# Performance work log

Measured on AMD Instinct MI355X. Metric: run time of the kernel, lower is better.

The kernel has to match this reference:

```python
import jax, jax.numpy as jnp
from jax import lax
import numpy as np

RADIUS = 0.2   # ball-query radius (module init arg)
NSAMPLE = 32   # gather_size
STRIDE = 4     # npoint = ceil(N / STRIDE)


def setup_inputs() -> dict:
    key = jax.random.key(0)
    k1, k2, k3 = jax.random.split(key, 3)
    points = jax.random.uniform(k1, (4, 8192, 3), jnp.float32)      # (B,N,3) in unit cube
    features = jax.random.normal(k2, (4, 8192, 64), jnp.float32)    # (B,N,C)
    # Conv2d(in=C+3, out=128, kernel=(1, NSAMPLE), bias=False) weight
    weight = jax.random.normal(k3, (128, 67, 1, 32), jnp.float32) * 0.02
    return {"points": points, "features": features, "weight": weight}


def fps(xyz, npoint):
    """Furthest point sampling. xyz: (B,N,3) -> inds (B,npoint) int32."""
    B, N, _ = xyz.shape
    start = jnp.zeros((B,), jnp.int32)          # standard FPS starts at index 0
    dist0 = jnp.full((B, N), 1e10, xyz.dtype)

    def body(carry, _):
        dist, last = carry
        last_xyz = jnp.take_along_axis(xyz, last[:, None, None], axis=1)  # (B,1,3)
        d = jnp.sum((xyz - last_xyz) ** 2, axis=-1)                        # (B,N)
        dist = jnp.minimum(dist, d)
        nxt = jnp.argmax(dist, axis=-1).astype(jnp.int32)
        return (dist, nxt), nxt

    (_, _), rest = lax.scan(body, (dist0, start), None, length=npoint - 1)
    return jnp.concatenate([start[None, :], rest], axis=0).T  # (B,npoint)


def ball_query(xyz, new_xyz, radius, nsample):
    """For each center, first `nsample` point indices within radius, padded with
    the first valid index (pointnet2 semantics). Returns (B,npoint,nsample)."""
    N = xyz.shape[1]
    d2 = jnp.sum((new_xyz[:, :, None, :] - xyz[:, None, :, :]) ** 2, axis=-1)  # (B,npoint,N)
    cand = jnp.where(d2 < radius * radius, jnp.arange(N, dtype=jnp.int32), N)
    neg, _ = lax.top_k(-cand, nsample)   # smallest nsample indices, in order
    idx = -neg
    first = idx[..., :1]                 # center itself is always in-ball -> valid
    return jnp.where(idx == N, first, idx)


def _forward(points, features, weight):
    B, N, _ = points.shape
    npoint = (N + STRIDE - 1) // STRIDE
    inds = fps(points, npoint)                                        # (B,npoint)
    new_xyz = jnp.take_along_axis(points, inds[..., None], axis=1)    # (B,npoint,3)
    idx = ball_query(points, new_xyz, RADIUS, NSAMPLE)                # (B,npoint,nsample)

    gather = lambda v: jax.vmap(lambda a, i: a[i])(v, idx)            # (B,npoint,nsample,*)
    g_xyz = gather(points) - new_xyz[:, :, None, :]                   # relative coords
    g_feat = gather(features)
    g = jnp.concatenate([g_xyz, g_feat], axis=-1)                     # (B,npoint,nsample,3+C)

    # Conv2d with kernel (1,nsample): contract over channel + neighbor axes.
    conv = jnp.einsum("bpsc,ocs->bpo", g, weight[:, :, 0, :])         # (B,npoint,Cout)
    return new_xyz, conv


def reference(points, features, weight):
    return _forward(points, features, weight)
```

## Files before the change

kernel.cpp:

```cpp
#include <hip/hip_runtime.h>

#define BATCH   4
#define NPTS    8192
#define NPOINT  2048
#define NSAMPLE 32
#define NCH     67
#define NOUT    128
#define NP      4
#define FPS_T   512
#define NWAVE   (FPS_T / 64)
#define KPT     (NPTS / FPS_T)
#define NBKT    64

#define DPP_ROW_SHR1    0x111
#define DPP_ROW_SHR2    0x112
#define DPP_ROW_SHR4    0x114
#define DPP_ROW_SHR8    0x118
#define DPP_ROW_BCAST15 0x142
#define DPP_ROW_BCAST31 0x143

#define DPP_MAX_HOP(key, ctrl)                                                 \
    {                                                                          \
        int _lo = (int)(unsigned)(key);                                        \
        int _hi = (int)(unsigned)((key) >> 32);                                \
        int _olo = __builtin_amdgcn_update_dpp(0, _lo, (ctrl), 0xF, 0xF, true);\
        int _ohi = __builtin_amdgcn_update_dpp(0, _hi, (ctrl), 0xF, 0xF, true);\
        unsigned long long _o =                                                \
            ((unsigned long long)(unsigned)_ohi << 32) | (unsigned)_olo;       \
        if (_o > (key)) (key) = _o;                                            \
    }

#define DPP_REDUCE_MAX(key)            \
    DPP_MAX_HOP(key, DPP_ROW_SHR1);    \
    DPP_MAX_HOP(key, DPP_ROW_SHR2);    \
    DPP_MAX_HOP(key, DPP_ROW_SHR4);    \
    DPP_MAX_HOP(key, DPP_ROW_SHR8);    \
    DPP_MAX_HOP(key, DPP_ROW_BCAST15); \
    DPP_MAX_HOP(key, DPP_ROW_BCAST31);

__global__ __launch_bounds__(FPS_T) void fps_kernel(
    const float* __restrict__ points, float* __restrict__ new_xyz)
{
#pragma clang fp contract(off)
    const int b    = blockIdx.x;
    const int t    = threadIdx.x;
    const int lane = t & 63;
    const int w    = t >> 6;
    const float* pts = points + (size_t)b * NPTS * 3;

    __shared__ float2 xy[NPTS];
    __shared__ float2 zd[NPTS];
    __shared__ unsigned short orig16[NPTS];
    __shared__ unsigned long long key_g[2][NBKT];
    __shared__ int start[NBKT + 1];
    __shared__ int cursor[NBKT];
    __shared__ float bbr[6][NWAVE];

    float mnx = 1e30f, mny = 1e30f, mnz = 1e30f;
    float mxx = -1e30f, mxy = -1e30f, mxz = -1e30f;
    for (int k = 0; k < KPT; ++k) {
        const int i = k * FPS_T + t;
        float xx = pts[3 * i], yy = pts[3 * i + 1], zz = pts[3 * i + 2];
        mnx = fminf(mnx, xx); mxx = fmaxf(mxx, xx);
        mny = fminf(mny, yy); mxy = fmaxf(mxy, yy);
        mnz = fminf(mnz, zz); mxz = fmaxf(mxz, zz);
    }
#pragma unroll
    for (int off = 32; off >= 1; off >>= 1) {
        mnx = fminf(mnx, __shfl_down(mnx, off));
        mny = fminf(mny, __shfl_down(mny, off));
        mnz = fminf(mnz, __shfl_down(mnz, off));
        mxx = fmaxf(mxx, __shfl_down(mxx, off));
        mxy = fmaxf(mxy, __shfl_down(mxy, off));
        mxz = fmaxf(mxz, __shfl_down(mxz, off));
    }
    if (lane == 0) {
        bbr[0][w] = mnx; bbr[1][w] = mny; bbr[2][w] = mnz;
        bbr[3][w] = mxx; bbr[4][w] = mxy; bbr[5][w] = mxz;
    }
    if (t < NBKT) cursor[t] = 0;
    __syncthreads();
    mnx = bbr[0][0]; mny = bbr[1][0]; mnz = bbr[2][0];
    mxx = bbr[3][0]; mxy = bbr[4][0]; mxz = bbr[5][0];
#pragma unroll
    for (int q = 1; q < NWAVE; ++q) {
        mnx = fminf(mnx, bbr[0][q]); mny = fminf(mny, bbr[1][q]);
        mnz = fminf(mnz, bbr[2][q]); mxx = fmaxf(mxx, bbr[3][q]);
        mxy = fmaxf(mxy, bbr[4][q]); mxz = fmaxf(mxz, bbr[5][q]);
    }
    const float rx = mxx - mnx, ry = mxy - mny, rz = mxz - mnz;
    const float sclx = (rx > 0.f) ? 4.0f / rx : 0.f;
    const float scly = (ry > 0.f) ? 4.0f / ry : 0.f;
    const float sclz = (rz > 0.f) ? 4.0f / rz : 0.f;

    for (int k = 0; k < KPT; ++k) {
        const int i = k * FPS_T + t;
        float xx = pts[3 * i], yy = pts[3 * i + 1], zz = pts[3 * i + 2];
        int cxi = min(3, max(0, (int)((xx - mnx) * sclx)));
        int cyi = min(3, max(0, (int)((yy - mny) * scly)));
        int czi = min(3, max(0, (int)((zz - mnz) * sclz)));
        atomicAdd(&cursor[cxi | (cyi << 2) | (czi << 4)], 1);
    }
    __syncthreads();
    if (t == 0) {
        int acc = 0;
        for (int g = 0; g < NBKT; ++g) { start[g] = acc; acc += cursor[g]; }
        start[NBKT] = acc;
    }
    __syncthreads();
    const int vs0 = start[lane];
    const int vln = start[lane + 1] - vs0;
    if (t < NBKT) cursor[t] = start[t];
    __syncthreads();

    for (int k = 0; k < KPT; ++k) {
        const int i = k * FPS_T + t;
        float xx = pts[3 * i], yy = pts[3 * i + 1], zz = pts[3 * i + 2];
        int cxi = min(3, max(0, (int)((xx - mnx) * sclx)));
        int cyi = min(3, max(0, (int)((yy - mny) * scly)));
        int czi = min(3, max(0, (int)((zz - mnz) * sclz)));
        int slot = atomicAdd(&cursor[cxi | (cyi << 2) | (czi << 4)], 1);
        xy[slot] = make_float2(xx, yy);
        zd[slot] = make_float2(zz, 10000000000.0f);
        orig16[slot] = (unsigned short)i;
    }

    const float cwx = rx * 0.25f, cwy = ry * 0.25f, cwz = rz * 0.25f;
    const float bxl = mnx + (float)(lane & 3) * cwx,        bxh = bxl + cwx;
    const float byl = mny + (float)((lane >> 2) & 3) * cwy, byh = byl + cwy;
    const float bzl = mnz + (float)((lane >> 4) & 3) * cwz, bzh = bzl + cwz;
    const unsigned long long below = (1ull << lane) - 1ull;

    float cx = pts[0], cy = pts[1], cz = pts[2];
    if (t == 0) {
        float* o = new_xyz + (size_t)b * NPOINT * 3;
        o[0] = cx; o[1] = cy; o[2] = cz;
    }
    unsigned long long kk =
        ((unsigned long long)__float_as_uint(10000000000.0f) << 32);
    __syncthreads();

    for (int it = 1; it < NPOINT; ++it) {
        const int par = it & 1;

        float ddx = fmaxf(fmaxf(bxl - cx, cx - bxh), 0.0f);
        float ddy = fmaxf(fmaxf(byl - cy, cy - byh), 0.0f);
        float ddz = fmaxf(fmaxf(bzl - cz, cz - bzh), 0.0f);
        float dmin2 = ddx * ddx + ddy * ddy + ddz * ddz;
        float ub = __uint_as_float((unsigned)(kk >> 32));
        bool scan = dmin2 < ub * 1.0001f + 1e-5f;
        unsigned long long m = __ballot(scan);

        const int rank = (int)__popcll(m & below);
        const bool mine = scan && ((rank & (NWAVE - 1)) == w);
        unsigned long long mw = __ballot(mine);

        while (mw) {
            const int g = __ffsll((long long)mw) - 1;
            mw &= mw - 1;
            const int s0 = __builtin_amdgcn_readlane(vs0, g);
            const int ln = __builtin_amdgcn_readlane(vln, g);
            unsigned long long bk = 0;
            for (int jo = lane; jo < ln; jo += 64) {
                const int j = s0 + jo;
                float2 vxy = xy[j];
                float2 vzd = zd[j];
                float dx = vxy.x - cx;
                float dy = vxy.y - cy;
                float dz = vzd.x - cz;
                float d  = ((dx * dx) + (dy * dy)) + (dz * dz);
                float nd = fminf(vzd.y, d);
                zd[j].y = nd;
                unsigned long long kkey =
                    ((unsigned long long)__float_as_uint(nd) << 32)
                  | ((unsigned)(8191 - (int)orig16[j]) << 13)
                  | (unsigned)j;
                if (kkey > bk) bk = kkey;
            }
            DPP_REDUCE_MAX(bk);
            if (lane == 63) key_g[par][g] = bk;
        }
        __syncthreads();

        if (scan) kk = key_g[par][lane];
        unsigned long long rr = kk;
        DPP_REDUCE_MAX(rr);
        const unsigned rlo =
            (unsigned)__builtin_amdgcn_readlane((int)(unsigned)rr, 63);
        const int slot = (int)(rlo & 0x1FFFu);
        float2 wxy = xy[slot];
        float2 wzd = zd[slot];
        cx = wxy.x; cy = wxy.y; cz = wzd.x;
        if (t == 0) {
            float* o = new_xyz + ((size_t)b * NPOINT + it) * 3;
            o[0] = cx; o[1] = cy; o[2] = cz;
        }
    }
}

__global__ __launch_bounds__(256) void ballq_kernel(
    const float* __restrict__ points, const float* __restrict__ new_xyz,
    int* __restrict__ ballidx)
{
#pragma clang fp contract(off)
    const int wid  = (int)((blockIdx.x * 256 + threadIdx.x) >> 6);
    const int lane = threadIdx.x & 63;
    const int b = wid / NPOINT;
    const float* ctr = new_xyz + (size_t)wid * 3;
    const float cx = ctr[0], cy = ctr[1], cz = ctr[2];
    const float* pts = points + (size_t)b * NPTS * 3;
    int* out = ballidx + (size_t)wid * NSAMPLE;
    const float r2 = (float)(0.2 * 0.2);

    int cnt = 0;
    int first = 0;
    bool havefirst = false;
    for (int base = 0; base < NPTS && cnt < NSAMPLE; base += 64) {
        const int j = base + lane;
        float dx = pts[3 * j + 0] - cx;
        float dy = pts[3 * j + 1] - cy;
        float dz = pts[3 * j + 2] - cz;
        float d2 = ((dx * dx) + (dy * dy)) + (dz * dz);
        const bool in = d2 < r2;
        unsigned long long m = __ballot(in);
        if (in) {
            int pos = cnt + __popcll(m & ((1ull << lane) - 1ull));
            if (pos < NSAMPLE) out[pos] = j;
        }
        if (!havefirst && m != 0ull) {
            first = base + (__ffsll((long long)m) - 1);
            havefirst = true;
        }
        cnt += __popcll(m);
    }
    if (lane >= cnt && lane < NSAMPLE) out[lane] = first;
}

__global__ __launch_bounds__(128) void conv_kernel(
    const float* __restrict__ points, const float* __restrict__ features,
    const float* __restrict__ weight, const float* __restrict__ new_xyz,
    const int* __restrict__ ballidx, float* __restrict__ conv_out)
{
    __shared__ float g[NP][NCH][NSAMPLE];
    const int t = threadIdx.x;
    const int bp0 = blockIdx.x * NP;
    const int b = bp0 / NPOINT;
    const float* pts = points + (size_t)b * NPTS * 3;
    const float* fts = features + (size_t)b * NPTS * 64;

    {
        const int p = t >> 5;
        const int s = t & 31;
        const int ci = bp0 + p;
        const int j = ballidx[(size_t)ci * NSAMPLE + s];
        const float* ctr = new_xyz + (size_t)ci * 3;
        const float* pj = pts + 3 * j;
        g[p][0][s] = pj[0] - ctr[0];
        g[p][1][s] = pj[1] - ctr[1];
        g[p][2][s] = pj[2] - ctr[2];
        const float4* fj = (const float4*)(fts + (size_t)j * 64);
#pragma unroll
        for (int c4 = 0; c4 < 16; ++c4) {
            float4 v = fj[c4];
            g[p][3 + 4 * c4 + 0][s] = v.x;
            g[p][3 + 4 * c4 + 1][s] = v.y;
            g[p][3 + 4 * c4 + 2][s] = v.z;
            g[p][3 + 4 * c4 + 3][s] = v.w;
        }
    }
    __syncthreads();

    const int o = t;
    float acc0 = 0.f, acc1 = 0.f, acc2 = 0.f, acc3 = 0.f;
    const float* wr = weight + (size_t)o * NCH * NSAMPLE;
    for (int c = 0; c < NCH; ++c) {
        const float4* w4 = (const float4*)(wr + c * NSAMPLE);
#pragma unroll
        for (int s4 = 0; s4 < 8; ++s4) {
            float4 wv = w4[s4];
            float4 g0 = *(const float4*)&g[0][c][s4 * 4];
            float4 g1 = *(const float4*)&g[1][c][s4 * 4];
            float4 g2 = *(const float4*)&g[2][c][s4 * 4];
            float4 g3 = *(const float4*)&g[3][c][s4 * 4];
            acc0 += g0.x * wv.x + g0.y * wv.y + g0.z * wv.z + g0.w * wv.w;
            acc1 += g1.x * wv.x + g1.y * wv.y + g1.z * wv.z + g1.w * wv.w;
            acc2 += g2.x * wv.x + g2.y * wv.y + g2.z * wv.z + g2.w * wv.w;
            acc3 += g3.x * wv.x + g3.y * wv.y + g3.z * wv.z + g3.w * wv.w;
        }
    }
    float* outp = conv_out + (size_t)bp0 * NOUT;
    outp[0 * NOUT + o] = acc0;
    outp[1 * NOUT + o] = acc1;
    outp[2 * NOUT + o] = acc2;
    outp[3 * NOUT + o] = acc3;
}

extern "C" void kernel_launch(void* const* d_in, const int* in_sizes, int n_in,
                              void* d_out, int out_size, void* d_ws, size_t ws_size,
                              hipStream_t stream)
{
    const float* points   = (const float*)d_in[0];
    const float* features = (const float*)d_in[1];
    const float* weight   = (const float*)d_in[2];

    float* new_xyz = (float*)d_out;
    float* conv    = (float*)d_out + (size_t)BATCH * NPOINT * 3;

    int* ballidx = (int*)d_ws;

    fps_kernel<<<BATCH, FPS_T, 0, stream>>>(points, new_xyz);
    ballq_kernel<<<(BATCH * NPOINT * 64) / 256, 256, 0, stream>>>(points, new_xyz, ballidx);
    conv_kernel<<<(BATCH * NPOINT) / NP, 128, 0, stream>>>(points, features, weight, new_xyz, ballidx, conv);
}
```

Measured before the change: 2.018 ms.

## Fuse FPS, ball query and conv into one persistent kernel with progress flags

Merges the three kernels into a single persistent launch. Four blocks run furthest point sampling and publish progress counters every 16 centers. The remaining blocks pull tickets and spin on those counters, so ball query and conv for finished centers overlap with the sequential FPS loop. Ball indices now stay in shared memory instead of a global workspace. The cost is a spin-wait protocol that relies on all blocks being co-resident and on correct release/acquire ordering, plus a memset launch.

```diff
diff --git a/kernel.cpp b/kernel.cpp
--- a/kernel.cpp
+++ b/kernel.cpp
@@ -6,11 +6,14 @@
 #define NSAMPLE 32
 #define NCH     67
 #define NOUT    128
-#define NP      4
 #define FPS_T   512
 #define NWAVE   (FPS_T / 64)
 #define KPT     (NPTS / FPS_T)
 #define NBKT    64
+#define NFPS    4
+#define NBLK    256
+#define TPT     8
+#define NTICK   (BATCH * NPOINT / TPT)
 
 #define DPP_ROW_SHR1    0x111
 #define DPP_ROW_SHR2    0x112
@@ -38,261 +41,277 @@
     DPP_MAX_HOP(key, DPP_ROW_BCAST15); \
     DPP_MAX_HOP(key, DPP_ROW_BCAST31);
 
-__global__ __launch_bounds__(FPS_T) void fps_kernel(
-    const float* __restrict__ points, float* __restrict__ new_xyz)
+__global__ __launch_bounds__(FPS_T) void fused_kernel(
+    const float* __restrict__ points, const float* __restrict__ features,
+    const float* __restrict__ weight, float* __restrict__ new_xyz,
+    float* __restrict__ conv_out, int* __restrict__ ctl)
 {
-#pragma clang fp contract(off)
-    const int b    = blockIdx.x;
+    __shared__ __attribute__((aligned(16))) char smem[149504];
     const int t    = threadIdx.x;
     const int lane = t & 63;
     const int w    = t >> 6;
-    const float* pts = points + (size_t)b * NPTS * 3;
-
-    __shared__ float2 xy[NPTS];
-    __shared__ float2 zd[NPTS];
-    __shared__ unsigned short orig16[NPTS];
-    __shared__ unsigned long long key_g[2][NBKT];
-    __shared__ int start[NBKT + 1];
-    __shared__ int cursor[NBKT];
-    __shared__ float bbr[6][NWAVE];
-
-    float mnx = 1e30f, mny = 1e30f, mnz = 1e30f;
-    float mxx = -1e30f, mxy = -1e30f, mxz = -1e30f;
-    for (int k = 0; k < KPT; ++k) {
-        const int i = k * FPS_T + t;
-        float xx = pts[3 * i], yy = pts[3 * i + 1], zz = pts[3 * i + 2];
-        mnx = fminf(mnx, xx); mxx = fmaxf(mxx, xx);
-        mny = fminf(mny, yy); mxy = fmaxf(mxy, yy);
-        mnz = fminf(mnz, zz); mxz = fmaxf(mxz, zz);
+    int* prog = ctl;
+    int* ticket = ctl + 32;
+
+    if (blockIdx.x < NFPS) {
+#pragma clang fp contract(off)
+        const int b = blockIdx.x;
+        const float* pts = points + (size_t)b * NPTS * 3;
+
+        float2* xy = (float2*)smem;
+        float2* zd = (float2*)(smem + 65536);
+        unsigned short* orig16 = (unsigned short*)(smem + 131072);
+        unsigned long long (*key_g)[NBKT] =
+            (unsigned long long (*)[NBKT])(smem + 147456);
+        int* start  = (int*)(smem + 148480);
+        int* cursor = (int*)(smem + 148744);
+        float (*bbr)[NWAVE] = (float (*)[NWAVE])(smem + 149000);
+
+        float mnx = 1e30f, mny = 1e30f, mnz = 1e30f;
+        float mxx = -1e30f, mxy = -1e30f, mxz = -1e30f;
+        for (int k = 0; k < KPT; ++k) {
+            const int i = k * FPS_T + t;
+            float xx = pts[3 * i], yy = pts[3 * i + 1], zz = pts[3 * i + 2];
+            mnx = fminf(mnx, xx); mxx = fmaxf(mxx, xx);
+            mny = fminf(mny, yy); mxy = fmaxf(mxy, yy);
+            mnz = fminf(mnz, zz); mxz = fmaxf(mxz, zz);
+        }
+#pragma unroll
+        for (int off = 32; off >= 1; off >>= 1) {
+            mnx = fminf(mnx, __shfl_down(mnx, off));
+            mny = fminf(mny, __shfl_down(mny, off));
+            mnz = fminf(mnz, __shfl_down(mnz, off));
+            mxx = fmaxf(mxx, __shfl_down(mxx, off));
+            mxy = fmaxf(mxy, __shfl_down(mxy, off));
+            mxz = fmaxf(mxz, __shfl_down(mxz, off));
+        }
+        if (lane == 0) {
+            bbr[0][w] = mnx; bbr[1][w] = mny; bbr[2][w] = mnz;
+            bbr[3][w] = mxx; bbr[4][w] = mxy; bbr[5][w] = mxz;
+        }
+        if (t < NBKT) cursor[t] = 0;
+        __syncthreads();
+        mnx = bbr[0][0]; mny = bbr[1][0]; mnz = bbr[2][0];
+        mxx = bbr[3][0]; mxy = bbr[4][0]; mxz = bbr[5][0];
+#pragma unroll
+        for (int q = 1; q < NWAVE; ++q) {
+            mnx = fminf(mnx, bbr[0][q]); mny = fminf(mny, bbr[1][q]);
+            mnz = fminf(mnz, bbr[2][q]); mxx = fmaxf(mxx, bbr[3][q]);
+            mxy = fmaxf(mxy, bbr[4][q]); mxz = fmaxf(mxz, bbr[5][q]);
+        }
+        const float rx = mxx - mnx, ry = mxy - mny, rz = mxz - mnz;
+        const float sclx = (rx > 0.f) ? 4.0f / rx : 0.f;
+        const float scly = (ry > 0.f) ? 4.0f / ry : 0.f;
+        const float sclz = (rz > 0.f) ? 4.0f / rz : 0.f;
+
+        for (int k = 0; k < KPT; ++k) {
+            const int i = k * FPS_T + t;
+            float xx = pts[3 * i], yy = pts[3 * i + 1], zz = pts[3 * i + 2];
+            int cxi = min(3, max(0, (int)((xx - mnx) * sclx)));
+            int cyi = min(3, max(0, (int)((yy - mny) * scly)));
+            int czi = min(3, max(0, (int)((zz - mnz) * sclz)));
+            atomicAdd(&cursor[cxi | (cyi << 2) | (czi << 4)], 1);
+        }
+        __syncthreads();
+        if (t == 0) {
+            int acc = 0;
+            for (int g = 0; g < NBKT; ++g) { start[g] = acc; acc += cursor[g]; }
+            start[NBKT] = acc;
+        }
+        __syncthreads();
+        const int vs0 = start[lane];
+        const int vln = start[lane + 1] - vs0;
+        if (t < NBKT) cursor[t] = start[t];
+        __syncthreads();
+
+        for (int k = 0; k < KPT; ++k) {
+            const int i = k * FPS_T + t;
+            float xx = pts[3 * i], yy = pts[3 * i + 1], zz = pts[3 * i + 2];
+            int cxi = min(3, max(0, (int)((xx - mnx) * sclx)));
+            int cyi = min(3, max(0, (int)((yy - mny) * scly)));
+            int czi = min(3, max(0, (int)((zz - mnz) * sclz)));
+            int slot = atomicAdd(&cursor[cxi | (cyi << 2) | (czi << 4)], 1);
+            xy[slot] = make_float2(xx, yy);
+            zd[slot] = make_float2(zz, 10000000000.0f);
+            orig16[slot] = (unsigned short)i;
+        }
+
+        const float cwx = rx * 0.25f, cwy = ry * 0.25f, cwz = rz * 0.25f;
+        const float bxl = mnx + (float)(lane & 3) * cwx,        bxh = bxl + cwx;
+        const float byl = mny + (float)((lane >> 2) & 3) * cwy, byh = byl + cwy;
+        const float bzl = mnz + (float)((lane >> 4) & 3) * cwz, bzh = bzl + cwz;
+        const unsigned long long below = (1ull << lane) - 1ull;
+
+        float cx = pts[0], cy = pts[1], cz = pts[2];
+        if (t == 0) {
+            float* o = new_xyz + (size_t)b * NPOINT * 3;
+            o[0] = cx; o[1] = cy; o[2] = cz;
+        }
+        unsigned long long kk =
+            ((unsigned long long)__float_as_uint(10000000000.0f) << 32);
+        __syncthreads();
+
+        for (int it = 1; it < NPOINT; ++it) {
+            const int par = it & 1;
+            float ddx = fmaxf(fmaxf(bxl - cx, cx - bxh), 0.0f);
+            float ddy = fmaxf(fmaxf(byl - cy, cy - byh), 0.0f);
+            float ddz = fmaxf(fmaxf(bzl - cz, cz - bzh), 0.0f);
+            float dmin2 = ddx * ddx + ddy * ddy + ddz * ddz;
+            float ub = __uint_as_float((unsigned)(kk >> 32));
+            bool scan = dmin2 < ub * 1.0001f + 1e-5f;
+            unsigned long long m = __ballot(scan);
+
+            const int rank = (int)__popcll(m & below);
+            const bool mine = scan && ((rank & (NWAVE - 1)) == w);
+            unsigned long long mw = __ballot(mine);
+
+            while (mw) {
+                const int g = __ffsll((long long)mw) - 1;
+                mw &= mw - 1;
+                const int s0 = __builtin_amdgcn_readlane(vs0, g);
+                const int ln = __builtin_amdgcn_readlane(vln, g);
+                unsigned long long bk = 0;
+                for (int jo = lane; jo < ln; jo += 64) {
+                    const int j = s0 + jo;
+                    float2 vxy = xy[j];
+                    float2 vzd = zd[j];
+                    float dx = vxy.x - cx;
+                    float dy = vxy.y - cy;
+                    float dz = vzd.x - cz;
+                    float d  = ((dx * dx) + (dy * dy)) + (dz * dz);
+                    float nd = fminf(vzd.y, d);
+                    zd[j].y = nd;
+                    unsigned long long kkey =
+                        ((unsigned long long)__float_as_uint(nd) << 32)
+                      | ((unsigned)(8191 - (int)orig16[j]) << 13)
+                      | (unsigned)j;
+                    if (kkey > bk) bk = kkey;
+                }
+                DPP_REDUCE_MAX(bk);
+                if (lane == 63) key_g[par][g] = bk;
+            }
+            __syncthreads();
+
+            if (scan) kk = key_g[par][lane];
+            unsigned long long rr = kk;
+            DPP_REDUCE_MAX(rr);
+            const unsigned rlo =
+                (unsigned)__builtin_amdgcn_readlane((int)(unsigned)rr, 63);
+            const int slot = (int)(rlo & 0x1FFFu);
+            float2 wxy = xy[slot];
+            float2 wzd = zd[slot];
+            cx = wxy.x; cy = wxy.y; cz = wzd.x;
+            if (t == 0) {
+                float* o = new_xyz + ((size_t)b * NPOINT + it) * 3;
+                o[0] = cx; o[1] = cy; o[2] = cz;
+                if (((it & 15) == 15) || (it == NPOINT - 1)) {
+                    __threadfence();
+                    __hip_atomic_store(&prog[b], it + 1, __ATOMIC_RELEASE,
+                                       __HIP_MEMORY_SCOPE_AGENT);
+                }
+            }
+        }
+        return;
     }
+
+    float (*g)[NCH][NSAMPLE] = (float (*)[NCH][NSAMPLE])smem;
+    int (*idx)[NSAMPLE] = (int (*)[NSAMPLE])(smem + 68608);
+    int* tk_s = (int*)(smem + 69632);
+
+    for (;;) {
+        if (t == 0) *tk_s = atomicAdd(ticket, 1);
+        __syncthreads();
+        const int T = *tk_s;
+        __syncthreads();
+        if (T >= NTICK) break;
+        const int b   = T & 3;
+        const int it0 = (T >> 2) * TPT;
+
+        if (t == 0) {
+            while (__hip_atomic_load(&prog[b], __ATOMIC_ACQUIRE,
+                                     __HIP_MEMORY_SCOPE_AGENT) < it0 + TPT)
+                __builtin_amdgcn_s_sleep(8);
+        }
+        __syncthreads();
+
+        const float* pts = points + (size_t)b * NPTS * 3;
+        const float* fts = features + (size_t)b * NPTS * 64;
+
+        {
+#pragma clang fp contract(off)
+            const int gci = b * NPOINT + it0 + w;
+            const float cx = new_xyz[3 * gci + 0];
+            const float cy = new_xyz[3 * gci + 1];
+            const float cz = new_xyz[3 * gci + 2];
+            const float r2 = (float)(0.2 * 0.2);
+            int* out = idx[w];
+            int cnt = 0, first = 0;
+            bool havefirst = false;
+            for (int base = 0; base < NPTS && cnt < NSAMPLE; base += 64) {
+                const int j = base + lane;
+                float dx = pts[3 * j + 0] - cx;
+                float dy = pts[3 * j + 1] - cy;
+                float dz = pts[3 * j + 2] - cz;
+                float d2 = ((dx * dx) + (dy * dy)) + (dz * dz);
+                const bool in = d2 < r2;
+                unsigned long long m = __ballot(in);
+                if (in) {
+                    int pos = cnt + __popcll(m & ((1ull << lane) - 1ull));
+                    if (pos < NSAMPLE) out[pos] = j;
+                }
+                if (!havefirst && m != 0ull) {
+                    first = base + (__ffsll((long long)m) - 1);
+                    havefirst = true;
+                }
+                cnt += __popcll(m);
+            }
+            if (lane >= cnt && lane < NSAMPLE) out[lane] = first;
+        }
+        __syncthreads();
+
+        if (t < TPT * NSAMPLE) {
+            const int p = t >> 5;
+            const int s = t & 31;
+            const int gci = b * NPOINT + it0 + p;
+            const int j = idx[p][s];
+            const float* pj = pts + 3 * j;
+            g[p][0][s] = pj[0] - new_xyz[3 * gci + 0];
+            g[p][1][s] = pj[1] - new_xyz[3 * gci + 1];
+            g[p][2][s] = pj[2] - new_xyz[3 * gci + 2];
+            const float4* fj = (const float4*)(fts + (size_t)j * 64);
 #pragma unroll
-    for (int off = 32; off >= 1; off >>= 1) {
-        mnx = fminf(mnx, __shfl_down(mnx, off));
-        mny = fminf(mny, __shfl_down(mny, off));
-        mnz = fminf(mnz, __shfl_down(mnz, off));
-        mxx = fmaxf(mxx, __shfl_down(mxx, off));
-        mxy = fmaxf(mxy, __shfl_down(mxy, off));
-        mxz = fmaxf(mxz, __shfl_down(mxz, off));
+            for (int c4 = 0; c4 < 16; ++c4) {
+                float4 v = fj[c4];
+                g[p][3 + 4 * c4 + 0][s] = v.x;
+                g[p][3 + 4 * c4 + 1][s] = v.y;
+                g[p][3 + 4 * c4 + 2][s] = v.z;
+                g[p][3 + 4 * c4 + 3][s] = v.w;
+            }
+        }
+        __syncthreads();
+
+        {
+            const int o = t & 127;
+            const int q = t >> 7;
+            float acc0 = 0.f, acc1 = 0.f;
+            const float* wr = weight + (size_t)o * NCH * NSAMPLE;
+            for (int c = 0; c < NCH; ++c) {
+                const float4* w4 = (const float4*)(wr + c * NSAMPLE);
+#pragma unroll
+                for (int s4 = 0; s4 < 8; ++s4) {
+                    float4 wv = w4[s4];
+                    float4 g0 = *(const float4*)&g[q][c][s4 * 4];
+                    float4 g1 = *(const float4*)&g[q + 4][c][s4 * 4];
+                    acc0 += g0.x * wv.x + g0.y * wv.y + g0.z * wv.z + g0.w * wv.w;
+                    acc1 += g1.x * wv.x + g1.y * wv.y + g1.z * wv.z + g1.w * wv.w;
+                }
+            }
+            float* outp = conv_out + ((size_t)b * NPOINT + it0) * NOUT;
+            outp[(q    ) * NOUT + o] = acc0;
+            outp[(q + 4) * NOUT + o] = acc1;
+        }
+        __syncthreads();
     }
-    if (lane == 0) {
-        bbr[0][w] = mnx; bbr[1][w] = mny; bbr[2][w] = mnz;
-        bbr[3][w] = mxx; bbr[4][w] = mxy; bbr[5][w] = mxz;
-    }
-    if (t < NBKT) cursor[t] = 0;
-    __syncthreads();
-    mnx = bbr[0][0]; mny = bbr[1][0]; mnz = bbr[2][0];
-    mxx = bbr[3][0]; mxy = bbr[4][0]; mxz = bbr[5][0];
-#pragma unroll
-    for (int q = 1; q < NWAVE; ++q) {
-        mnx = fminf(mnx, bbr[0][q]); mny = fminf(mny, bbr[1][q]);
-        mnz = fminf(mnz, bbr[2][q]); mxx = fmaxf(mxx, bbr[3][q]);
-        mxy = fmaxf(mxy, bbr[4][q]); mxz = fmaxf(mxz, bbr[5][q]);
-    }
-    const float rx = mxx - mnx, ry = mxy - mny, rz = mxz - mnz;
-    const float sclx = (rx > 0.f) ? 4.0f / rx : 0.f;
-    const float scly = (ry > 0.f) ? 4.0f / ry : 0.f;
-    const float sclz = (rz > 0.f) ? 4.0f / rz : 0.f;
-
-    for (int k = 0; k < KPT; ++k) {
-        const int i = k * FPS_T + t;
-        float xx = pts[3 * i], yy = pts[3 * i + 1], zz = pts[3 * i + 2];
-        int cxi = min(3, max(0, (int)((xx - mnx) * sclx)));
-        int cyi = min(3, max(0, (int)((yy - mny) * scly)));
-        int czi = min(3, max(0, (int)((zz - mnz) * sclz)));
-        atomicAdd(&cursor[cxi | (cyi << 2) | (czi << 4)], 1);
-    }
-    __syncthreads();
-    if (t == 0) {
-        int acc = 0;
-        for (int g = 0; g < NBKT; ++g) { start[g] = acc; acc += cursor[g]; }
-        start[NBKT] = acc;
-    }
-    __syncthreads();
-    const int vs0 = start[lane];
-    const int vln = start[lane + 1] - vs0;
-    if (t < NBKT) cursor[t] = start[t];
-    __syncthreads();
-
-    for (int k = 0; k < KPT; ++k) {
-        const int i = k * FPS_T + t;
-        float xx = pts[3 * i], yy = pts[3 * i + 1], zz = pts[3 * i + 2];
-        int cxi = min(3, max(0, (int)((xx - mnx) * sclx)));
-        int cyi = min(3, max(0, (int)((yy - mny) * scly)));
-        int czi = min(3, max(0, (int)((zz - mnz) * sclz)));
-        int slot = atomicAdd(&cursor[cxi | (cyi << 2) | (czi << 4)], 1);
-        xy[slot] = make_float2(xx, yy);
-        zd[slot] = make_float2(zz, 10000000000.0f);
-        orig16[slot] = (unsigned short)i;
-    }
-
-    const float cwx = rx * 0.25f, cwy = ry * 0.25f, cwz = rz * 0.25f;
-    const float bxl = mnx + (float)(lane & 3) * cwx,        bxh = bxl + cwx;
-    const float byl = mny + (float)((lane >> 2) & 3) * cwy, byh = byl + cwy;
-    const float bzl = mnz + (float)((lane >> 4) & 3) * cwz, bzh = bzl + cwz;
-    const unsigned long long below = (1ull << lane) - 1ull;
-
-    float cx = pts[0], cy = pts[1], cz = pts[2];
-    if (t == 0) {
-        float* o = new_xyz + (size_t)b * NPOINT * 3;
-        o[0] = cx; o[1] = cy; o[2] = cz;
-    }
-    unsigned long long kk =
-        ((unsigned long long)__float_as_uint(10000000000.0f) << 32);
-    __syncthreads();
-
-    for (int it = 1; it < NPOINT; ++it) {
-        const int par = it & 1;
-
-        float ddx = fmaxf(fmaxf(bxl - cx, cx - bxh), 0.0f);
-        float ddy = fmaxf(fmaxf(byl - cy, cy - byh), 0.0f);
-        float ddz = fmaxf(fmaxf(bzl - cz, cz - bzh), 0.0f);
-        float dmin2 = ddx * ddx + ddy * ddy + ddz * ddz;
-        float ub = __uint_as_float((unsigned)(kk >> 32));
-        bool scan = dmin2 < ub * 1.0001f + 1e-5f;
-        unsigned long long m = __ballot(scan);
-
-        const int rank = (int)__popcll(m & below);
-        const bool mine = scan && ((rank & (NWAVE - 1)) == w);
-        unsigned long long mw = __ballot(mine);
-
-        while (mw) {
-            const int g = __ffsll((long long)mw) - 1;
-            mw &= mw - 1;
-            const int s0 = __builtin_amdgcn_readlane(vs0, g);
-            const int ln = __builtin_amdgcn_readlane(vln, g);
-            unsigned long long bk = 0;
-            for (int jo = lane; jo < ln; jo += 64) {
-                const int j = s0 + jo;
-                float2 vxy = xy[j];
-                float2 vzd = zd[j];
-                float dx = vxy.x - cx;
-                float dy = vxy.y - cy;
-                float dz = vzd.x - cz;
-                float d  = ((dx * dx) + (dy * dy)) + (dz * dz);
-                float nd = fminf(vzd.y, d);
-                zd[j].y = nd;
-                unsigned long long kkey =
-                    ((unsigned long long)__float_as_uint(nd) << 32)
-                  | ((unsigned)(8191 - (int)orig16[j]) << 13)
-                  | (unsigned)j;
-                if (kkey > bk) bk = kkey;
-            }
-            DPP_REDUCE_MAX(bk);
-            if (lane == 63) key_g[par][g] = bk;
-        }
-        __syncthreads();
-
-        if (scan) kk = key_g[par][lane];
-        unsigned long long rr = kk;
-        DPP_REDUCE_MAX(rr);
-        const unsigned rlo =
-            (unsigned)__builtin_amdgcn_readlane((int)(unsigned)rr, 63);
-        const int slot = (int)(rlo & 0x1FFFu);
-        float2 wxy = xy[slot];
-        float2 wzd = zd[slot];
-        cx = wxy.x; cy = wxy.y; cz = wzd.x;
-        if (t == 0) {
-            float* o = new_xyz + ((size_t)b * NPOINT + it) * 3;
-            o[0] = cx; o[1] = cy; o[2] = cz;
-        }
-    }
-}
-
-__global__ __launch_bounds__(256) void ballq_kernel(
-    const float* __restrict__ points, const float* __restrict__ new_xyz,
-    int* __restrict__ ballidx)
-{
-#pragma clang fp contract(off)
-    const int wid  = (int)((blockIdx.x * 256 + threadIdx.x) >> 6);
-    const int lane = threadIdx.x & 63;
-    const int b = wid / NPOINT;
-    const float* ctr = new_xyz + (size_t)wid * 3;
-    const float cx = ctr[0], cy = ctr[1], cz = ctr[2];
-    const float* pts = points + (size_t)b * NPTS * 3;
-    int* out = ballidx + (size_t)wid * NSAMPLE;
-    const float r2 = (float)(0.2 * 0.2);
-
-    int cnt = 0;
-    int first = 0;
-    bool havefirst = false;
-    for (int base = 0; base < NPTS && cnt < NSAMPLE; base += 64) {
-        const int j = base + lane;
-        float dx = pts[3 * j + 0] - cx;
-        float dy = pts[3 * j + 1] - cy;
-        float dz = pts[3 * j + 2] - cz;
-        float d2 = ((dx * dx) + (dy * dy)) + (dz * dz);
-        const bool in = d2 < r2;
-        unsigned long long m = __ballot(in);
-        if (in) {
-            int pos = cnt + __popcll(m & ((1ull << lane) - 1ull));
-            if (pos < NSAMPLE) out[pos] = j;
-        }
-        if (!havefirst && m != 0ull) {
-            first = base + (__ffsll((long long)m) - 1);
-            havefirst = true;
-        }
-        cnt += __popcll(m);
-    }
-    if (lane >= cnt && lane < NSAMPLE) out[lane] = first;
-}
-
-__global__ __launch_bounds__(128) void conv_kernel(
-    const float* __restrict__ points, const float* __restrict__ features,
-    const float* __restrict__ weight, const float* __restrict__ new_xyz,
-    const int* __restrict__ ballidx, float* __restrict__ conv_out)
-{
-    __shared__ float g[NP][NCH][NSAMPLE];
-    const int t = threadIdx.x;
-    const int bp0 = blockIdx.x * NP;
-    const int b = bp0 / NPOINT;
-    const float* pts = points + (size_t)b * NPTS * 3;
-    const float* fts = features + (size_t)b * NPTS * 64;
-
-    {
-        const int p = t >> 5;
-        const int s = t & 31;
-        const int ci = bp0 + p;
-        const int j = ballidx[(size_t)ci * NSAMPLE + s];
-        const float* ctr = new_xyz + (size_t)ci * 3;
-        const float* pj = pts + 3 * j;
-        g[p][0][s] = pj[0] - ctr[0];
-        g[p][1][s] = pj[1] - ctr[1];
-        g[p][2][s] = pj[2] - ctr[2];
-        const float4* fj = (const float4*)(fts + (size_t)j * 64);
-#pragma unroll
-        for (int c4 = 0; c4 < 16; ++c4) {
-            float4 v = fj[c4];
-            g[p][3 + 4 * c4 + 0][s] = v.x;
-            g[p][3 + 4 * c4 + 1][s] = v.y;
-            g[p][3 + 4 * c4 + 2][s] = v.z;
-            g[p][3 + 4 * c4 + 3][s] = v.w;
-        }
-    }
-    __syncthreads();
-
-    const int o = t;
-    float acc0 = 0.f, acc1 = 0.f, acc2 = 0.f, acc3 = 0.f;
-    const float* wr = weight + (size_t)o * NCH * NSAMPLE;
-    for (int c = 0; c < NCH; ++c) {
-        const float4* w4 = (const float4*)(wr + c * NSAMPLE);
-#pragma unroll
-        for (int s4 = 0; s4 < 8; ++s4) {
-            float4 wv = w4[s4];
-            float4 g0 = *(const float4*)&g[0][c][s4 * 4];
-            float4 g1 = *(const float4*)&g[1][c][s4 * 4];
-            float4 g2 = *(const float4*)&g[2][c][s4 * 4];
-            float4 g3 = *(const float4*)&g[3][c][s4 * 4];
-            acc0 += g0.x * wv.x + g0.y * wv.y + g0.z * wv.z + g0.w * wv.w;
-            acc1 += g1.x * wv.x + g1.y * wv.y + g1.z * wv.z + g1.w * wv.w;
-            acc2 += g2.x * wv.x + g2.y * wv.y + g2.z * wv.z + g2.w * wv.w;
-            acc3 += g3.x * wv.x + g3.y * wv.y + g3.z * wv.z + g3.w * wv.w;
-        }
-    }
-    float* outp = conv_out + (size_t)bp0 * NOUT;
-    outp[0 * NOUT + o] = acc0;
-    outp[1 * NOUT + o] = acc1;
-    outp[2 * NOUT + o] = acc2;
-    outp[3 * NOUT + o] = acc3;
 }
 
 extern "C" void kernel_launch(void* const* d_in, const int* in_sizes, int n_in,
@@ -305,10 +324,9 @@
 
     float* new_xyz = (float*)d_out;
     float* conv    = (float*)d_out + (size_t)BATCH * NPOINT * 3;
-
-    int* ballidx = (int*)d_ws;
-
-    fps_kernel<<<BATCH, FPS_T, 0, stream>>>(points, new_xyz);
-    ballq_kernel<<<(BATCH * NPOINT * 64) / 256, 256, 0, stream>>>(points, new_xyz, ballidx);
-    conv_kernel<<<(BATCH * NPOINT) / NP, 128, 0, stream>>>(points, features, weight, new_xyz, ballidx, conv);
+    int* ctl = (int*)d_ws;
+
+    hipMemsetAsync(d_ws, 0, 256, stream);
+    fused_kernel<<<NBLK, FPS_T, 0, stream>>>(points, features, weight,
+                                             new_xyz, conv, ctl);
 }
```

Result: no change. 1.999 ms (-1.0%).
